# Performance work log

Hardware: AMD Instinct MI355X
Metric: run time of the kernel (lower is better)

The kernel has to match this reference:

```python
import jax, jax.numpy as jnp
import numpy as np

HIDDEN = 1024
QDIM = 16
B, S = 4, 2048
EPS = 1e-8


def setup_inputs() -> dict:
    key = jax.random.key(0)
    ks = jax.random.split(key, 12)
    sc_h = 1.0 / np.sqrt(HIDDEN)
    inp = {
        "x": jax.random.normal(ks[0], (B, S, HIDDEN), dtype=jnp.float32),
        "Wq": jax.random.normal(ks[1], (HIDDEN, HIDDEN), dtype=jnp.float32) * sc_h,
        "bq": jnp.zeros((HIDDEN,), dtype=jnp.float32),
        "Wk": jax.random.normal(ks[2], (HIDDEN, HIDDEN), dtype=jnp.float32) * sc_h,
        "bk": jnp.zeros((HIDDEN,), dtype=jnp.float32),
        "Wv": jax.random.normal(ks[3], (HIDDEN, HIDDEN), dtype=jnp.float32) * sc_h,
        "bv": jnp.zeros((HIDDEN,), dtype=jnp.float32),
        "We": jax.random.normal(ks[4], (HIDDEN, QDIM), dtype=jnp.float32) * sc_h,
        "be": jnp.zeros((QDIM,), dtype=jnp.float32),
        "Wo": jax.random.normal(ks[5], (HIDDEN, HIDDEN), dtype=jnp.float32) * sc_h,
        "bo": jnp.zeros((HIDDEN,), dtype=jnp.float32),
    }
    return inp


def _quantum_embed(h, We, be):
    # Linear projection to quantum amplitude space, then normalize to a unit state.
    z = h @ We + be                     # [..., QDIM]
    nrm = jnp.sqrt(jnp.sum(z * z, axis=-1, keepdims=True) + EPS)
    return z / nrm


def reference(x, Wq, bq, Wk, bk, Wv, bv, We, be, Wo, bo):
    # Projections
    q = x @ Wq + bq                     # [B,S,H]
    k = x @ Wk + bk
    v = x @ Wv + bv
    # Quantum state embeddings (unit-normalized amplitudes)
    q_q = _quantum_embed(q, We, be)     # [B,S,QDIM]
    k_q = _quantum_embed(k, We, be)
    # Quantum fidelity similarity |<q|k>|^2, vectorized over all pairs
    ov = jnp.einsum("bqd,bkd->bqk", q_q, k_q)   # [B,S,S]
    attn = jax.nn.softmax(ov * ov, axis=-1)
    attended = jnp.einsum("bqk,bkh->bqh", attn, v)
    return attended @ Wo + bo
```

## Files before the change

### kernel.cpp

```cpp
#include <hip/hip_runtime.h>

#define H 1024
#define QD 16
#define BATCH 4
#define SEQ 2048
#define MROWS 8192

typedef __bf16 bf16x8 __attribute__((ext_vector_type(8)));
typedef __bf16 bf16x4 __attribute__((ext_vector_type(4)));
typedef float f32x4 __attribute__((ext_vector_type(4)));

__device__ __forceinline__ void async_g2l_16(const void* g, void* l) {
  __builtin_amdgcn_global_load_lds(
      (const __attribute__((address_space(1))) unsigned int*)g,
      (__attribute__((address_space(3))) unsigned int*)l, 16, 0, 0);
}

__global__ __launch_bounds__(256) void cvt_split(const float* __restrict__ src,
                                                 __bf16* __restrict__ hi,
                                                 __bf16* __restrict__ lo, int n) {
  int i = (blockIdx.x * 256 + threadIdx.x) * 4;
  if (i < n) {
    float4 f = *(const float4*)(src + i);
    bf16x4 h, l;
    h[0] = (__bf16)f.x; l[0] = (__bf16)(f.x - (float)h[0]);
    h[1] = (__bf16)f.y; l[1] = (__bf16)(f.y - (float)h[1]);
    h[2] = (__bf16)f.z; l[2] = (__bf16)(f.z - (float)h[2]);
    h[3] = (__bf16)f.w; l[3] = (__bf16)(f.w - (float)h[3]);
    *(bf16x4*)(hi + i) = h;
    *(bf16x4*)(lo + i) = l;
  }
}

__global__ __launch_bounds__(256) void transpose_cvt_f32_bf16(
    const float* __restrict__ src, __bf16* __restrict__ dst, int R, int C) {
  __shared__ float t[32][33];
  const int rb = blockIdx.y * 32, cb = blockIdx.x * 32;
  const int c = threadIdx.x & 31;
  const int r0 = threadIdx.x >> 5;
#pragma unroll
  for (int rr = r0; rr < 32; rr += 8)
    t[rr][c] = src[(long)(rb + rr) * C + cb + c];
  __syncthreads();
#pragma unroll
  for (int rr = r0; rr < 32; rr += 8)
    dst[(long)(cb + rr) * R + rb + c] = (__bf16)t[c][rr];
}

__global__ __launch_bounds__(256) void k2_cqk(const float* __restrict__ Wq,
                                              const float* __restrict__ Wk,
                                              const float* __restrict__ We,
                                              __bf16* __restrict__ Cth,
                                              __bf16* __restrict__ Ctl) {
  const int gw = blockIdx.x * 4 + (threadIdx.x >> 6);
  const int lane = threadIdx.x & 63;
  const int mat = gw & 1, k = gw >> 1;
  const float* Wrow = (mat ? Wk : Wq) + (long)k * H;
  const int col = lane & 15, q4 = lane >> 4;
  float acc = 0.f;
  for (int n0 = 0; n0 < 256; ++n0) {
    int n = q4 * 256 + n0;
    acc += Wrow[n] * We[n * QD + col];
  }
  acc += __shfl_xor(acc, 16);
  acc += __shfl_xor(acc, 32);
  if (lane < 16) {
    __bf16 hi = (__bf16)acc;
    __bf16 lo = (__bf16)(acc - (float)hi);
    long idx = (long)(mat * 16 + col) * H + k;
    Cth[idx] = hi;
    Ctl[idx] = lo;
  }
}

__global__ void k2b_dvec(const float* __restrict__ bq, const float* __restrict__ bk,
                         const float* __restrict__ We, const float* __restrict__ be,
                         float* __restrict__ dvec) {
  int j = threadIdx.x;
  if (j < 32) {
    int mat = j >> 4, col = j & 15;
    const float* b = mat ? bk : bq;
    float acc = be[col];
    for (int n = 0; n < H; ++n) acc += b[n] * We[n * QD + col];
    dvec[j] = acc;
  }
}

__global__ __launch_bounds__(256) void k3_embed_mfma(
    const __bf16* __restrict__ xh, const __bf16* __restrict__ xl,
    const __bf16* __restrict__ Cth, const __bf16* __restrict__ Ctl,
    const float* __restrict__ dvec, __bf16* __restrict__ qq32,
    __bf16* __restrict__ kk32) {
  __shared__ __bf16 Ah[32 * 64];
  __shared__ __bf16 Al[32 * 64];
  __shared__ __bf16 Bh[32 * 64];
  __shared__ __bf16 Bl[32 * 64];
  const int tid = threadIdx.x;
  const int lane = tid & 63;
  const int w = tid >> 6;
  const int rowhalf = w >> 1;
  const int ntile = w & 1;
  const int l15 = lane & 15, quad = lane >> 4;
  const long rowBase = (long)blockIdx.x * 32;

  const int srow = tid >> 3;
  const int segsw = ((tid & 7) ^ (srow & 7)) * 8;
  const __bf16* agh = xh + (rowBase + srow) * H + segsw;
  const __bf16* agl = xl + (rowBase + srow) * H + segsw;
  const __bf16* bgh = Cth + (long)srow * H + segsw;
  const __bf16* bgl = Ctl + (long)srow * H + segsw;
  __bf16* lah = &Ah[srow * 64 + (tid & 7) * 8];
  __bf16* lal = &Al[srow * 64 + (tid & 7) * 8];
  __bf16* lbh = &Bh[srow * 64 + (tid & 7) * 8];
  __bf16* lbl = &Bl[srow * 64 + (tid & 7) * 8];

  f32x4 acc;
  acc[0] = 0.f; acc[1] = 0.f; acc[2] = 0.f; acc[3] = 0.f;
  const int arow = (rowhalf * 16 + l15) * 64;
  const int brow = (ntile * 16 + l15) * 64;
  const int h7 = l15 & 7;

  for (int k0 = 0; k0 < H; k0 += 64) {
    async_g2l_16(agh + k0, lah);
    async_g2l_16(agl + k0, lal);
    async_g2l_16(bgh + k0, lbh);
    async_g2l_16(bgl + k0, lbl);
    __syncthreads();
#pragma unroll
    for (int s = 0; s < 2; ++s) {
      const int slot = ((s * 4 + quad) ^ h7) * 8;
      bf16x8 fah = *(const bf16x8*)&Ah[arow + slot];
      bf16x8 fal = *(const bf16x8*)&Al[arow + slot];
      bf16x8 fbh = *(const bf16x8*)&Bh[brow + slot];
      bf16x8 fbl = *(const bf16x8*)&Bl[brow + slot];
      acc = __builtin_amdgcn_mfma_f32_16x16x32_bf16(fah, fbh, acc, 0, 0, 0);
      acc = __builtin_amdgcn_mfma_f32_16x16x32_bf16(fal, fbh, acc, 0, 0, 0);
      acc = __builtin_amdgcn_mfma_f32_16x16x32_bf16(fah, fbl, acc, 0, 0, 0);
    }
    __syncthreads();
  }

  const float dv = dvec[ntile * 16 + l15];
  __bf16* outp = ntile ? kk32 : qq32;
#pragma unroll
  for (int r = 0; r < 4; ++r) {
    float z = acc[r] + dv;
    float s2 = z * z;
    s2 += __shfl_xor(s2, 1);
    s2 += __shfl_xor(s2, 2);
    s2 += __shfl_xor(s2, 4);
    s2 += __shfl_xor(s2, 8);
    float val = z * rsqrtf(s2 + 1e-8f);
    long row = rowBase + rowhalf * 16 + quad * 4 + r;
    outp[row * 32 + l15] = (__bf16)val;
    outp[row * 32 + 16 + l15] = (__bf16)0.f;
  }
}

#define PSTR 136
__global__ __launch_bounds__(512) void fused_attn(
    const __bf16* __restrict__ qq32, const __bf16* __restrict__ kk32,
    const __bf16* __restrict__ v_t, __bf16* __restrict__ attn) {
  __shared__ __bf16 Plds[128 * PSTR];
  __shared__ __bf16 Vlds[256 * 128];
  __shared__ float rsum2[128 * 2];
  const int tid = threadIdx.x;
  const int lane = tid & 63;
  const int w = tid >> 6;
  const int l15 = lane & 15, quad = lane >> 4;
  const int ws_k = w & 1, ws_q = w >> 1;
  const int wp_h = w & 3, wp_q = w >> 2;
  const int b = blockIdx.z;
  const long qbase = (long)blockIdx.y * 128;
  const long hbase = (long)blockIdx.x * 256;

  bf16x8 bq[2];
  {
    const __bf16* qqp =
        qq32 + ((long)b * SEQ + qbase + ws_q * 32 + l15) * 32 + quad * 8;
#pragma unroll
    for (int n = 0; n < 2; ++n) bq[n] = *(const bf16x8*)(qqp + (long)n * 16 * 32);
  }
  const __bf16* kkb = kk32 + ((long)b * SEQ + ws_k * 64 + l15) * 32 + quad * 8;

  const int vrow = tid >> 4;
  const int vseg = tid & 15;
  const __bf16* vg = v_t + (long)b * H * SEQ + (hbase + vrow) * SEQ +
                     ((vseg ^ (vrow & 15)) * 8);
  __bf16* vl = &Vlds[vrow * 128 + vseg * 8];

  f32x4 acc[4][4];
#pragma unroll
  for (int i = 0; i < 4; ++i)
#pragma unroll
    for (int j = 0; j < 4; ++j) {
      acc[i][j][0] = 0.f; acc[i][j][1] = 0.f; acc[i][j][2] = 0.f; acc[i][j][3] = 0.f;
    }
  float rsPart[2] = {0.f, 0.f};

  bf16x8 ak[4];
#pragma unroll
  for (int i = 0; i < 4; ++i) ak[i] = *(const bf16x8*)(kkb + (long)(i * 16) * 32);

  for (int k0 = 0; k0 < SEQ; k0 += 128) {
#pragma unroll
    for (int j = 0; j < 8; ++j)
      async_g2l_16(vg + (long)k0 + (long)(j * 32) * SEQ, vl + j * 32 * 128);

#pragma unroll
    for (int i = 0; i < 4; ++i) {
#pragma unroll
      for (int n = 0; n < 2; ++n) {
        f32x4 s;
        s[0] = 0.f; s[1] = 0.f; s[2] = 0.f; s[3] = 0.f;
        s = __builtin_amdgcn_mfma_f32_16x16x32_bf16(ak[i], bq[n], s, 0, 0, 0);
        bf16x4 pw;
        float part = 0.f;
#pragma unroll
        for (int r = 0; r < 4; ++r) {
          float wgt = __expf(s[r] * s[r]);
          part += wgt;
          pw[r] = (__bf16)wgt;
        }
        rsPart[n] += part;
        *(bf16x4*)&Plds[(ws_q * 32 + n * 16 + l15) * PSTR + ws_k * 64 + i * 16 +
                        quad * 4] = pw;
      }
    }
    if (k0 + 128 < SEQ) {
#pragma unroll
      for (int i = 0; i < 4; ++i)
        ak[i] = *(const bf16x8*)(kkb + (long)(k0 + 128 + i * 16) * 32);
    }
    __syncthreads();
#pragma unroll
    for (int ks = 0; ks < 4; ++ks) {
      bf16x8 ap[4], bv[4];
#pragma unroll
      for (int i = 0; i < 4; ++i)
        ap[i] = *(const bf16x8*)&Plds[(wp_q * 64 + i * 16 + l15) * PSTR +
                                      ks * 32 + quad * 8];
#pragma unroll
      for (int j = 0; j < 4; ++j) {
        const int vr = wp_h * 64 + j * 16 + l15;
        const int slot = ((ks * 4 + quad) ^ l15) * 8;
        bv[j] = *(const bf16x8*)&Vlds[vr * 128 + slot];
      }
#pragma unroll
      for (int i = 0; i < 4; ++i)
#pragma unroll
        for (int j = 0; j < 4; ++j)
          acc[i][j] =
              __builtin_amdgcn_mfma_f32_16x16x32_bf16(ap[i], bv[j], acc[i][j], 0, 0, 0);
    }
    __syncthreads();
  }

#pragma unroll
  for (int n = 0; n < 2; ++n) {
    float vs = rsPart[n];
    vs += __shfl_xor(vs, 16);
    vs += __shfl_xor(vs, 32);
    if (lane < 16) rsum2[(ws_q * 32 + n * 16 + l15) * 2 + ws_k] = vs;
  }
  __syncthreads();

  float rinv[4][4];
#pragma unroll
  for (int i = 0; i < 4; ++i)
#pragma unroll
    for (int r = 0; r < 4; ++r) {
      int row = wp_q * 64 + i * 16 + quad * 4 + r;
      rinv[i][r] = 1.0f / (rsum2[row * 2] + rsum2[row * 2 + 1]);
    }

  __bf16* ob = attn + ((long)b * SEQ + qbase) * H + hbase;
#pragma unroll
  for (int i = 0; i < 4; ++i)
#pragma unroll
    for (int j = 0; j < 4; ++j) {
      const int colL = wp_h * 64 + j * 16 + l15;
#pragma unroll
      for (int r = 0; r < 4; ++r) {
        const int rowL = wp_q * 64 + i * 16 + quad * 4 + r;
        ob[(long)rowL * H + colL] = (__bf16)(acc[i][j][r] * rinv[i][r]);
      }
    }
}

template <int OUTMODE, int HASBIAS>
__global__ __launch_bounds__(256) void gemm_bt(
    const __bf16* __restrict__ A, const __bf16* __restrict__ Bt,
    void* __restrict__ Cout, const float* __restrict__ bias, int M, int N, int K) {
  __shared__ __bf16 Alds[128 * 64];
  __shared__ __bf16 Blds[128 * 64];
  const int tid = threadIdx.x;
  const int lane = tid & 63;
  const int w = tid >> 6;
  const int wm = w >> 1, wn = w & 1;
  const int l15 = lane & 15, quad = lane >> 4;
  const long rowBase = (long)blockIdx.y * 128;
  const long colBase = (long)blockIdx.x * 128;

  const int srow = lane >> 3;
  const int segsw = ((lane & 7) ^ srow) * 8;

  const __bf16* ag[4];
  const __bf16* bg[4];
  __bf16* as_[4];
  __bf16* bs_[4];
#pragma unroll
  for (int j = 0; j < 4; ++j) {
    int r = j * 32 + w * 8;
    ag[j] = A + (rowBase + r + srow) * (long)K + segsw;
    bg[j] = Bt + (colBase + r + srow) * (long)K + segsw;
    as_[j] = &Alds[r * 64 + (lane & 7) * 8];
    bs_[j] = &Blds[r * 64 + (lane & 7) * 8];
  }

  f32x4 acc[4][4];
#pragma unroll
  for (int i = 0; i < 4; ++i)
#pragma unroll
    for (int j = 0; j < 4; ++j) {
      acc[i][j][0] = 0.f; acc[i][j][1] = 0.f; acc[i][j][2] = 0.f; acc[i][j][3] = 0.f;
    }

  const int h7 = l15 & 7;

  for (int k0 = 0; k0 < K; k0 += 64) {
#pragma unroll
    for (int j = 0; j < 4; ++j) {
      async_g2l_16(ag[j], as_[j]);
      async_g2l_16(bg[j], bs_[j]);
      ag[j] += 64;
      bg[j] += 64;
    }
    __syncthreads();
#pragma unroll
    for (int s = 0; s < 2; ++s) {
      const int slot = ((s * 4 + quad) ^ h7) * 8;
      bf16x8 af[4], bfv[4];
#pragma unroll
      for (int i = 0; i < 4; ++i) {
        af[i] = *(const bf16x8*)&Alds[(wm * 64 + i * 16 + l15) * 64 + slot];
        bfv[i] = *(const bf16x8*)&Blds[(wn * 64 + i * 16 + l15) * 64 + slot];
      }
#pragma unroll
      for (int i = 0; i < 4; ++i)
#pragma unroll
        for (int j = 0; j < 4; ++j)
          acc[i][j] =
              __builtin_amdgcn_mfma_f32_16x16x32_bf16(af[i], bfv[j], acc[i][j], 0, 0, 0);
    }
    __syncthreads();
  }

  const long crow0 = rowBase + wm * 64 + quad * 4;
  const long ccol0 = colBase + wn * 64 + l15;
#pragma unroll
  for (int i = 0; i < 4; ++i) {
#pragma unroll
    for (int j = 0; j < 4; ++j) {
      long col = ccol0 + j * 16;
      float bb = HASBIAS ? bias[col] : 0.f;
      if (OUTMODE == 2) {
        long row0 = crow0 + i * 16;
        int bz = (int)(row0 >> 11);
        long rb = row0 & (SEQ - 1);
        bf16x4 pv;
#pragma unroll
        for (int r = 0; r < 4; ++r) pv[r] = (__bf16)(acc[i][j][r] + bb);
        *(bf16x4*)&((__bf16*)Cout)[((long)bz * N + col) * SEQ + rb] = pv;
      } else {
#pragma unroll
        for (int r = 0; r < 4; ++r) {
          long row = crow0 + i * 16 + r;
          float val = acc[i][j][r] + bb;
          if (OUTMODE == 0)
            ((float*)Cout)[row * N + col] = val;
          else
            ((__bf16*)Cout)[row * N + col] = (__bf16)val;
        }
      }
    }
  }
}

extern "C" void kernel_launch(void* const* d_in, const int* in_sizes, int n_in,
                              void* d_out, int out_size, void* d_ws, size_t ws_size,
                              hipStream_t stream) {
  const float* x = (const float*)d_in[0];
  const float* Wq = (const float*)d_in[1];
  const float* bq = (const float*)d_in[2];
  const float* Wk = (const float*)d_in[3];
  const float* bk = (const float*)d_in[4];
  const float* Wv = (const float*)d_in[5];
  const float* bv = (const float*)d_in[6];
  const float* We = (const float*)d_in[7];
  const float* be = (const float*)d_in[8];
  const float* Wo = (const float*)d_in[9];
  const float* bo = (const float*)d_in[10];
  float* out = (float*)d_out;

  char* ws = (char*)d_ws;
  size_t o = 0;
  auto alloc = [&](size_t n) {
    size_t r = o;
    o += (n + 255) & ~(size_t)255;
    return r;
  };
  __bf16* xbf = (__bf16*)(ws + alloc((size_t)MROWS * H * 2));
  __bf16* v_t = (__bf16*)(ws + alloc((size_t)MROWS * H * 2));
  __bf16* attn = (__bf16*)(ws + alloc((size_t)MROWS * H * 2));
  __bf16* Wvt = (__bf16*)(ws + alloc((size_t)H * H * 2));
  __bf16* Wot = (__bf16*)(ws + alloc((size_t)H * H * 2));
  __bf16* Cth = (__bf16*)(ws + alloc((size_t)32 * H * 2));
  __bf16* Ctl = (__bf16*)(ws + alloc((size_t)32 * H * 2));
  float* dvec = (float*)(ws + alloc(32 * 4));
  __bf16* qq32 = (__bf16*)(ws + alloc((size_t)MROWS * 32 * 2));
  __bf16* kk32 = (__bf16*)(ws + alloc((size_t)MROWS * 32 * 2));
  __bf16* xlo = attn;
  if (ws_size < o) return;

  cvt_split<<<MROWS * H / 1024, 256, 0, stream>>>(x, xbf, xlo, MROWS * H);
  transpose_cvt_f32_bf16<<<dim3(32, 32), 256, 0, stream>>>(Wv, Wvt, H, H);
  transpose_cvt_f32_bf16<<<dim3(32, 32), 256, 0, stream>>>(Wo, Wot, H, H);
  k2_cqk<<<512, 256, 0, stream>>>(Wq, Wk, We, Cth, Ctl);
  k2b_dvec<<<1, 64, 0, stream>>>(bq, bk, We, be, dvec);
  k3_embed_mfma<<<MROWS / 32, 256, 0, stream>>>(xbf, xlo, Cth, Ctl, dvec, qq32, kk32);
  gemm_bt<2, 1><<<dim3(8, 64), 256, 0, stream>>>(xbf, Wvt, v_t, bv, MROWS, H, H);
  fused_attn<<<dim3(4, 16, BATCH), 512, 0, stream>>>(qq32, kk32, v_t, attn);
  gemm_bt<0, 1><<<dim3(8, 64), 256, 0, stream>>>(attn, Wot, out, bo, MROWS, H, H);
}
```

Measured before the change: 258.4 us.

## Shrink attention tile, drop V LDS staging, use exp2 with prescaled Q

New measurement: 338.4 us. 1.31x slower.

```diff
diff --git a/kernel.cpp b/kernel.cpp
--- a/kernel.cpp
+++ b/kernel.cpp
@@ -141,6 +141,7 @@
   }
 
   const float dv = dvec[ntile * 16 + l15];
+  const float osc = ntile ? 1.0f : 1.20112240878f;
   __bf16* outp = ntile ? kk32 : qq32;
 #pragma unroll
   for (int r = 0; r < 4; ++r) {
@@ -150,29 +151,27 @@
     s2 += __shfl_xor(s2, 2);
     s2 += __shfl_xor(s2, 4);
     s2 += __shfl_xor(s2, 8);
-    float val = z * rsqrtf(s2 + 1e-8f);
+    float val = z * rsqrtf(s2 + 1e-8f) * osc;
     long row = rowBase + rowhalf * 16 + quad * 4 + r;
     outp[row * 32 + l15] = (__bf16)val;
     outp[row * 32 + 16 + l15] = (__bf16)0.f;
   }
 }
 
-#define PSTR 136
-__global__ __launch_bounds__(512) void fused_attn(
+__global__ __launch_bounds__(512, 4) void fused_attn(
     const __bf16* __restrict__ qq32, const __bf16* __restrict__ kk32,
     const __bf16* __restrict__ v_t, __bf16* __restrict__ attn) {
-  __shared__ __bf16 Plds[128 * PSTR];
-  __shared__ __bf16 Vlds[256 * 128];
-  __shared__ float rsum2[128 * 2];
+  __shared__ __bf16 Plds[64 * 128];
+  __shared__ float rsum4[64 * 4];
   const int tid = threadIdx.x;
   const int lane = tid & 63;
   const int w = tid >> 6;
   const int l15 = lane & 15, quad = lane >> 4;
-  const int ws_k = w & 1, ws_q = w >> 1;
+  const int ws_k = w & 3, ws_q = w >> 2;
   const int wp_h = w & 3, wp_q = w >> 2;
   const int b = blockIdx.z;
-  const long qbase = (long)blockIdx.y * 128;
-  const long hbase = (long)blockIdx.x * 256;
+  const long qbase = (long)blockIdx.x * 64;
+  const long hbase = (long)blockIdx.y * 256;
 
   bf16x8 bq[2];
   {
@@ -181,34 +180,25 @@
 #pragma unroll
     for (int n = 0; n < 2; ++n) bq[n] = *(const bf16x8*)(qqp + (long)n * 16 * 32);
   }
-  const __bf16* kkb = kk32 + ((long)b * SEQ + ws_k * 64 + l15) * 32 + quad * 8;
-
-  const int vrow = tid >> 4;
-  const int vseg = tid & 15;
-  const __bf16* vg = v_t + (long)b * H * SEQ + (hbase + vrow) * SEQ +
-                     ((vseg ^ (vrow & 15)) * 8);
-  __bf16* vl = &Vlds[vrow * 128 + vseg * 8];
-
-  f32x4 acc[4][4];
-#pragma unroll
-  for (int i = 0; i < 4; ++i)
+  const __bf16* kkb = kk32 + ((long)b * SEQ + ws_k * 32 + l15) * 32 + quad * 8;
+  const __bf16* vb = v_t + (long)b * H * SEQ + (hbase + wp_h * 64 + l15) * SEQ;
+
+  f32x4 acc[2][4];
+#pragma unroll
+  for (int i = 0; i < 2; ++i)
 #pragma unroll
     for (int j = 0; j < 4; ++j) {
       acc[i][j][0] = 0.f; acc[i][j][1] = 0.f; acc[i][j][2] = 0.f; acc[i][j][3] = 0.f;
     }
   float rsPart[2] = {0.f, 0.f};
 
-  bf16x8 ak[4];
-#pragma unroll
-  for (int i = 0; i < 4; ++i) ak[i] = *(const bf16x8*)(kkb + (long)(i * 16) * 32);
+  bf16x8 ak[2];
+#pragma unroll
+  for (int i = 0; i < 2; ++i) ak[i] = *(const bf16x8*)(kkb + (long)(i * 16) * 32);
 
   for (int k0 = 0; k0 < SEQ; k0 += 128) {
 #pragma unroll
-    for (int j = 0; j < 8; ++j)
-      async_g2l_16(vg + (long)k0 + (long)(j * 32) * SEQ, vl + j * 32 * 128);
-
-#pragma unroll
-    for (int i = 0; i < 4; ++i) {
+    for (int i = 0; i < 2; ++i) {
 #pragma unroll
       for (int n = 0; n < 2; ++n) {
         f32x4 s;
@@ -218,36 +208,35 @@
         float part = 0.f;
 #pragma unroll
         for (int r = 0; r < 4; ++r) {
-          float wgt = __expf(s[r] * s[r]);
+          float wgt = exp2f(s[r] * s[r]);
           part += wgt;
           pw[r] = (__bf16)wgt;
         }
         rsPart[n] += part;
-        *(bf16x4*)&Plds[(ws_q * 32 + n * 16 + l15) * PSTR + ws_k * 64 + i * 16 +
-                        quad * 4] = pw;
+        const int prow = ws_q * 32 + n * 16 + l15;
+        const int sl = (ws_k * 4 + i * 2 + (quad >> 1)) ^ l15;
+        *(bf16x4*)&Plds[prow * 128 + sl * 8 + (quad & 1) * 4] = pw;
       }
     }
     if (k0 + 128 < SEQ) {
 #pragma unroll
-      for (int i = 0; i < 4; ++i)
+      for (int i = 0; i < 2; ++i)
         ak[i] = *(const bf16x8*)(kkb + (long)(k0 + 128 + i * 16) * 32);
     }
     __syncthreads();
 #pragma unroll
     for (int ks = 0; ks < 4; ++ks) {
-      bf16x8 ap[4], bv[4];
-#pragma unroll
-      for (int i = 0; i < 4; ++i)
-        ap[i] = *(const bf16x8*)&Plds[(wp_q * 64 + i * 16 + l15) * PSTR +
-                                      ks * 32 + quad * 8];
-#pragma unroll
-      for (int j = 0; j < 4; ++j) {
-        const int vr = wp_h * 64 + j * 16 + l15;
-        const int slot = ((ks * 4 + quad) ^ l15) * 8;
-        bv[j] = *(const bf16x8*)&Vlds[vr * 128 + slot];
+      bf16x8 ap[2], bv[4];
+#pragma unroll
+      for (int i = 0; i < 2; ++i) {
+        const int prow = wp_q * 32 + i * 16 + l15;
+        ap[i] = *(const bf16x8*)&Plds[prow * 128 + (((ks * 4 + quad) ^ l15) * 8)];
       }
 #pragma unroll
-      for (int i = 0; i < 4; ++i)
+      for (int j = 0; j < 4; ++j)
+        bv[j] = *(const bf16x8*)(vb + (long)(j * 16) * SEQ + k0 + ks * 32 + quad * 8);
+#pragma unroll
+      for (int i = 0; i < 2; ++i)
 #pragma unroll
         for (int j = 0; j < 4; ++j)
           acc[i][j] =
@@ -261,28 +250,29 @@
     float vs = rsPart[n];
     vs += __shfl_xor(vs, 16);
     vs += __shfl_xor(vs, 32);
-    if (lane < 16) rsum2[(ws_q * 32 + n * 16 + l15) * 2 + ws_k] = vs;
+    if (lane < 16) rsum4[(ws_q * 32 + n * 16 + l15) * 4 + ws_k] = vs;
   }
   __syncthreads();
 
-  float rinv[4][4];
-#pragma unroll
-  for (int i = 0; i < 4; ++i)
+  float rinv[2][4];
+#pragma unroll
+  for (int i = 0; i < 2; ++i)
 #pragma unroll
     for (int r = 0; r < 4; ++r) {
-      int row = wp_q * 64 + i * 16 + quad * 4 + r;
-      rinv[i][r] = 1.0f / (rsum2[row * 2] + rsum2[row * 2 + 1]);
+      int row = wp_q * 32 + i * 16 + quad * 4 + r;
+      rinv[i][r] = 1.0f / (rsum4[row * 4] + rsum4[row * 4 + 1] +
+                           rsum4[row * 4 + 2] + rsum4[row * 4 + 3]);
     }
 
   __bf16* ob = attn + ((long)b * SEQ + qbase) * H + hbase;
 #pragma unroll
-  for (int i = 0; i < 4; ++i)
+  for (int i = 0; i < 2; ++i)
 #pragma unroll
     for (int j = 0; j < 4; ++j) {
       const int colL = wp_h * 64 + j * 16 + l15;
 #pragma unroll
       for (int r = 0; r < 4; ++r) {
-        const int rowL = wp_q * 64 + i * 16 + quad * 4 + r;
+        const int rowL = wp_q * 32 + i * 16 + quad * 4 + r;
         ob[(long)rowL * H + colL] = (__bf16)(acc[i][j][r] * rinv[i][r]);
       }
     }
@@ -430,6 +420,6 @@
   k2b_dvec<<<1, 64, 0, stream>>>(bq, bk, We, be, dvec);
   k3_embed_mfma<<<MROWS / 32, 256, 0, stream>>>(xbf, xlo, Cth, Ctl, dvec, qq32, kk32);
   gemm_bt<2, 1><<<dim3(8, 64), 256, 0, stream>>>(xbf, Wvt, v_t, bv, MROWS, H, H);
-  fused_attn<<<dim3(4, 16, BATCH), 512, 0, stream>>>(qq32, kk32, v_t, attn);
+  fused_attn<<<dim3(32, 4, BATCH), 512, 0, stream>>>(qq32, kk32, v_t, attn);
   gemm_bt<0, 1><<<dim3(8, 64), 256, 0, stream>>>(attn, Wot, out, bo, MROWS, H, H);
 }
```

## Triple-buffer V tiles and double-buffer P in fused attention with single barrier

Applied to the files above, without the earlier changes.

After: 256.8 us. Within noise of the previous version (-0.6%).

```diff
diff --git a/kernel.cpp b/kernel.cpp
--- a/kernel.cpp
+++ b/kernel.cpp
@@ -5,6 +5,7 @@
 #define BATCH 4
 #define SEQ 2048
 #define MROWS 8192
+#define KCH 64
 
 typedef __bf16 bf16x8 __attribute__((ext_vector_type(8)));
 typedef __bf16 bf16x4 __attribute__((ext_vector_type(4)));
@@ -141,6 +142,7 @@
   }
 
   const float dv = dvec[ntile * 16 + l15];
+  const float osc = ntile ? 1.0f : 1.20112240878f;
   __bf16* outp = ntile ? kk32 : qq32;
 #pragma unroll
   for (int r = 0; r < 4; ++r) {
@@ -150,19 +152,18 @@
     s2 += __shfl_xor(s2, 2);
     s2 += __shfl_xor(s2, 4);
     s2 += __shfl_xor(s2, 8);
-    float val = z * rsqrtf(s2 + 1e-8f);
+    float val = z * rsqrtf(s2 + 1e-8f) * osc;
     long row = rowBase + rowhalf * 16 + quad * 4 + r;
     outp[row * 32 + l15] = (__bf16)val;
     outp[row * 32 + 16 + l15] = (__bf16)0.f;
   }
 }
 
-#define PSTR 136
 __global__ __launch_bounds__(512) void fused_attn(
     const __bf16* __restrict__ qq32, const __bf16* __restrict__ kk32,
     const __bf16* __restrict__ v_t, __bf16* __restrict__ attn) {
-  __shared__ __bf16 Plds[128 * PSTR];
-  __shared__ __bf16 Vlds[256 * 128];
+  __shared__ __bf16 Vlds[3][256 * KCH];
+  __shared__ __bf16 Plds[2][128 * KCH];
   __shared__ float rsum2[128 * 2];
   const int tid = threadIdx.x;
   const int lane = tid & 63;
@@ -171,23 +172,21 @@
   const int ws_k = w & 1, ws_q = w >> 1;
   const int wp_h = w & 3, wp_q = w >> 2;
   const int b = blockIdx.z;
-  const long qbase = (long)blockIdx.y * 128;
-  const long hbase = (long)blockIdx.x * 256;
+  const long qbase = (long)blockIdx.x * 128;
+  const long hbase = (long)blockIdx.y * 256;
 
   bf16x8 bq[2];
   {
     const __bf16* qqp =
         qq32 + ((long)b * SEQ + qbase + ws_q * 32 + l15) * 32 + quad * 8;
-#pragma unroll
-    for (int n = 0; n < 2; ++n) bq[n] = *(const bf16x8*)(qqp + (long)n * 16 * 32);
-  }
-  const __bf16* kkb = kk32 + ((long)b * SEQ + ws_k * 64 + l15) * 32 + quad * 8;
-
-  const int vrow = tid >> 4;
-  const int vseg = tid & 15;
-  const __bf16* vg = v_t + (long)b * H * SEQ + (hbase + vrow) * SEQ +
-                     ((vseg ^ (vrow & 15)) * 8);
-  __bf16* vl = &Vlds[vrow * 128 + vseg * 8];
+    bq[0] = *(const bf16x8*)qqp;
+    bq[1] = *(const bf16x8*)(qqp + 16 * 32);
+  }
+  const __bf16* kkb = kk32 + ((long)b * SEQ + ws_k * 32 + l15) * 32 + quad * 8;
+
+  const int vR = tid >> 3;
+  const int vSL = (tid & 7) ^ (vR & 7);
+  const __bf16* vgbase = v_t + (long)b * H * SEQ + (hbase + vR) * SEQ + vSL * 8;
 
   f32x4 acc[4][4];
 #pragma unroll
@@ -198,17 +197,24 @@
     }
   float rsPart[2] = {0.f, 0.f};
 
-  bf16x8 ak[4];
-#pragma unroll
-  for (int i = 0; i < 4; ++i) ak[i] = *(const bf16x8*)(kkb + (long)(i * 16) * 32);
-
-  for (int k0 = 0; k0 < SEQ; k0 += 128) {
-#pragma unroll
-    for (int j = 0; j < 8; ++j)
-      async_g2l_16(vg + (long)k0 + (long)(j * 32) * SEQ, vl + j * 32 * 128);
-
-#pragma unroll
-    for (int i = 0; i < 4; ++i) {
+#pragma unroll
+  for (int j = 0; j < 4; ++j)
+    async_g2l_16(vgbase + (long)j * 64 * SEQ, &Vlds[0][j * 64 * KCH + tid * 8]);
+  bf16x8 ak[2];
+  ak[0] = *(const bf16x8*)kkb;
+  ak[1] = *(const bf16x8*)(kkb + 16 * 32);
+
+  int vcur = 0, vnxt = 1;
+  for (int t = 0; t < SEQ / KCH; ++t) {
+    const int kn = ((t + 1) & (SEQ / KCH - 1)) * KCH;
+#pragma unroll
+    for (int j = 0; j < 4; ++j)
+      async_g2l_16(vgbase + (long)j * 64 * SEQ + kn,
+                   &Vlds[vnxt][j * 64 * KCH + tid * 8]);
+
+    __bf16* Pw = Plds[t & 1];
+#pragma unroll
+    for (int i = 0; i < 2; ++i) {
 #pragma unroll
       for (int n = 0; n < 2; ++n) {
         f32x4 s;
@@ -218,33 +224,37 @@
         float part = 0.f;
 #pragma unroll
         for (int r = 0; r < 4; ++r) {
-          float wgt = __expf(s[r] * s[r]);
+          float wgt = exp2f(s[r] * s[r]);
           part += wgt;
           pw[r] = (__bf16)wgt;
         }
         rsPart[n] += part;
-        *(bf16x4*)&Plds[(ws_q * 32 + n * 16 + l15) * PSTR + ws_k * 64 + i * 16 +
-                        quad * 4] = pw;
-      }
-    }
-    if (k0 + 128 < SEQ) {
-#pragma unroll
-      for (int i = 0; i < 4; ++i)
-        ak[i] = *(const bf16x8*)(kkb + (long)(k0 + 128 + i * 16) * 32);
-    }
-    __syncthreads();
-#pragma unroll
-    for (int ks = 0; ks < 4; ++ks) {
+        const int q = ws_q * 32 + n * 16 + l15;
+        const int g = ws_k * 4 + i * 2 + (quad >> 1);
+        *(bf16x4*)&Pw[q * KCH + ((g ^ (q & 7)) << 3) + (quad & 1) * 4] = pw;
+      }
+    }
+    ak[0] = *(const bf16x8*)(kkb + (long)kn * 32);
+    ak[1] = *(const bf16x8*)(kkb + (long)(kn + 16) * 32);
+
+    asm volatile("s_waitcnt lgkmcnt(0)" ::: "memory");
+    asm volatile("s_waitcnt vmcnt(6)" ::: "memory");
+    __builtin_amdgcn_sched_barrier(0);
+    __builtin_amdgcn_s_barrier();
+
+    const __bf16* Vr = Vlds[vcur];
+#pragma unroll
+    for (int ks = 0; ks < 2; ++ks) {
       bf16x8 ap[4], bv[4];
 #pragma unroll
-      for (int i = 0; i < 4; ++i)
-        ap[i] = *(const bf16x8*)&Plds[(wp_q * 64 + i * 16 + l15) * PSTR +
-                                      ks * 32 + quad * 8];
+      for (int i = 0; i < 4; ++i) {
+        const int q = wp_q * 64 + i * 16 + l15;
+        ap[i] = *(const bf16x8*)&Pw[q * KCH + (((ks * 4 + quad) ^ (q & 7)) << 3)];
+      }
 #pragma unroll
       for (int j = 0; j < 4; ++j) {
         const int vr = wp_h * 64 + j * 16 + l15;
-        const int slot = ((ks * 4 + quad) ^ l15) * 8;
-        bv[j] = *(const bf16x8*)&Vlds[vr * 128 + slot];
+        bv[j] = *(const bf16x8*)&Vr[vr * KCH + (((ks * 4 + quad) ^ (vr & 7)) << 3)];
       }
 #pragma unroll
       for (int i = 0; i < 4; ++i)
@@ -253,7 +263,9 @@
           acc[i][j] =
               __builtin_amdgcn_mfma_f32_16x16x32_bf16(ap[i], bv[j], acc[i][j], 0, 0, 0);
     }
-    __syncthreads();
+    const int third = 3 - vcur - vnxt;
+    vcur = vnxt;
+    vnxt = third;
   }
 
 #pragma unroll
@@ -430,6 +442,6 @@
   k2b_dvec<<<1, 64, 0, stream>>>(bq, bk, We, be, dvec);
   k3_embed_mfma<<<MROWS / 32, 256, 0, stream>>>(xbf, xlo, Cth, Ctl, dvec, qq32, kk32);
   gemm_bt<2, 1><<<dim3(8, 64), 256, 0, stream>>>(xbf, Wvt, v_t, bv, MROWS, H, H);
-  fused_attn<<<dim3(4, 16, BATCH), 512, 0, stream>>>(qq32, kk32, v_t, attn);
+  fused_attn<<<dim3(16, 4, BATCH), 512, 0, stream>>>(qq32, kk32, v_t, attn);
   gemm_bt<0, 1><<<dim3(8, 64), 256, 0, stream>>>(attn, Wot, out, bo, MROWS, H, H);
 }
```
